# Kernel optimization log

Hardware: AMD Instinct MI355X
Metric: run time of the kernel (lower is better)

## Reference

```python
import jax, jax.numpy as jnp
import numpy as np

EMBED = 768
HEADS = 12
HEAD_DIM = EMBED // HEADS
HIDDEN = 4 * EMBED
EPS = 1e-5


def _layernorm(x, w, b):
    mu = jnp.mean(x, axis=-1, keepdims=True)
    var = jnp.mean(jnp.square(x - mu), axis=-1, keepdims=True)
    return (x - mu) * jax.lax.rsqrt(var + EPS) * w + b


def setup_inputs() -> dict:
    key = jax.random.key(0)
    ks = jax.random.split(key, 12)
    s = 0.02
    return {
        "x": jax.random.normal(ks[0], (2, 2048, EMBED), dtype=jnp.float32),
        "ln1_w": jnp.ones((EMBED,), jnp.float32),
        "ln1_b": jnp.zeros((EMBED,), jnp.float32),
        "qkv_w": jax.random.normal(ks[1], (3 * EMBED, EMBED), jnp.float32) * s,
        "qkv_b": jnp.zeros((3 * EMBED,), jnp.float32),
        "proj_w": jax.random.normal(ks[2], (EMBED, EMBED), jnp.float32) * s,
        "proj_b": jnp.zeros((EMBED,), jnp.float32),
        "ln2_w": jnp.ones((EMBED,), jnp.float32),
        "ln2_b": jnp.zeros((EMBED,), jnp.float32),
        "fc1_w": jax.random.normal(ks[3], (HIDDEN, EMBED), jnp.float32) * s,
        "fc1_b": jnp.zeros((HIDDEN,), jnp.float32),
        "fc2_w": jax.random.normal(ks[4], (EMBED, HIDDEN), jnp.float32) * s,
        "fc2_b": jnp.zeros((EMBED,), jnp.float32),
    }


def reference(x, ln1_w, ln1_b, qkv_w, qkv_b, proj_w, proj_b,
              ln2_w, ln2_b, fc1_w, fc1_b, fc2_w, fc2_b):
    B, N, C = x.shape
    scale = float(HEAD_DIM) ** 0.5  # NOTE: module MULTIPLIES by sqrt(head_dim)

    # --- attention branch ---
    h = _layernorm(x, ln1_w, ln1_b)
    qkv = h @ qkv_w.T + qkv_b                     # [B,N,3C]
    qkv = qkv.reshape(B, N, 3, HEADS, HEAD_DIM)
    q = qkv[:, :, 0].transpose(0, 2, 1, 3)        # [B,H,N,D]
    k = qkv[:, :, 1].transpose(0, 2, 1, 3)
    v = qkv[:, :, 2].transpose(0, 2, 1, 3)
    attn = jnp.einsum('bhnd,bhmd->bhnm', q, k) * scale
    attn = jax.nn.softmax(attn, axis=-1)
    o = jnp.einsum('bhnm,bhmd->bhnd', attn, v)    # [B,H,N,D]
    o = o.transpose(0, 2, 1, 3).reshape(B, N, C)
    x = x + (o @ proj_w.T + proj_b)

    # --- MLP branch ---
    h = _layernorm(x, ln2_w, ln2_b)
    h = jax.nn.gelu(h @ fc1_w.T + fc1_b, approximate=False)
    x = x + (h @ fc2_w.T + fc2_b)
    return x
```

## Files before the change

### kernel.cpp

```cpp
#include <hip/hip_runtime.h>
#include <hip/hip_bf16.h>

typedef __attribute__((ext_vector_type(8))) short short8;
typedef __attribute__((ext_vector_type(4))) float f32x4;
typedef __attribute__((ext_vector_type(4))) int i32x4;

__device__ inline unsigned short f2bs(float f) {
  union { float f; unsigned u; } v; v.f = f;
  unsigned r = v.u + 0x7fff + ((v.u >> 16) & 1);
  return (unsigned short)(r >> 16);
}

__device__ inline unsigned pkbf(float a, float b) {
  __hip_bfloat162 h = __float22bfloat162_rn(float2{a, b});
  union { __hip_bfloat162 h; unsigned u; } c; c.h = h;
  return c.u;
}

__device__ inline float exp2v(float x) {
  float r; asm("v_exp_f32 %0, %1" : "=v"(r) : "v"(x)); return r;
}

__device__ inline float max3f(float a, float b, float c) {
  return fmaxf(fmaxf(a, b), c);
}

__device__ inline void gload16(const void* g, void* l) {
  __builtin_amdgcn_global_load_lds((const __attribute__((address_space(1))) void*)g,
                                   (__attribute__((address_space(3))) void*)l,
                                   16, 0, 0);
}

__global__ __launch_bounds__(256)
void cvt_all(const float* __restrict__ s0, const float* __restrict__ s1,
             const float* __restrict__ s2, const float* __restrict__ s3,
             unsigned short* __restrict__ d0, unsigned short* __restrict__ d1,
             unsigned short* __restrict__ d2, unsigned short* __restrict__ d3)
{
  size_t i = (size_t)blockIdx.x * 256 + threadIdx.x;
  const float* src; unsigned short* dst;
  if (i < 442368) { src = s0; dst = d0; }
  else if (i < 589824) { src = s1; dst = d1; i -= 442368; }
  else if (i < 1179648) { src = s2; dst = d2; i -= 589824; }
  else { src = s3; dst = d3; i -= 1179648; }
  float4 v = ((const float4*)src)[i];
  ushort4 o;
  o.x = f2bs(v.x); o.y = f2bs(v.y); o.z = f2bs(v.z); o.w = f2bs(v.w);
  ((ushort4*)dst)[i] = o;
}

__global__ __launch_bounds__(256)
void ln_kernel(const float* __restrict__ x, const float* __restrict__ w,
               const float* __restrict__ bsh, unsigned short* __restrict__ out)
{
  const int row = blockIdx.x;
  const float* xr = x + (size_t)row * 768;
  float v[3];
  float s = 0.f, sq = 0.f;
#pragma unroll
  for (int i = 0; i < 3; ++i) {
    v[i] = xr[threadIdx.x + i * 256];
    s += v[i]; sq += v[i] * v[i];
  }
#pragma unroll
  for (int d = 1; d < 64; d <<= 1) {
    s  += __shfl_xor(s, d, 64);
    sq += __shfl_xor(sq, d, 64);
  }
  __shared__ float ss[4], ssq[4];
  const int wv = threadIdx.x >> 6;
  if ((threadIdx.x & 63) == 0) { ss[wv] = s; ssq[wv] = sq; }
  __syncthreads();
  s  = ss[0] + ss[1] + ss[2] + ss[3];
  sq = ssq[0] + ssq[1] + ssq[2] + ssq[3];
  const float mu = s * (1.0f / 768.0f);
  const float var = sq * (1.0f / 768.0f) - mu * mu;
  const float rstd = rsqrtf(var + 1e-5f);
#pragma unroll
  for (int i = 0; i < 3; ++i) {
    const int c = threadIdx.x + i * 256;
    out[(size_t)row * 768 + c] = f2bs((v[i] - mu) * rstd * w[c] + bsh[c]);
  }
}

__global__ __launch_bounds__(256)
void reduce_ln2(const float* __restrict__ p, const float* __restrict__ bias,
                const float* __restrict__ resid, const float* __restrict__ lw,
                const float* __restrict__ lb, float* __restrict__ x2,
                unsigned short* __restrict__ h)
{
  const size_t MN = 4096ull * 768;
  const int row = blockIdx.x;
  const size_t r0 = (size_t)row * 768;
  float v[3];
  float s = 0.f, sq = 0.f;
#pragma unroll
  for (int i = 0; i < 3; ++i) {
    const int c = threadIdx.x + i * 256;
    const float a = p[r0 + c] + p[MN + r0 + c] + bias[c] + resid[r0 + c];
    x2[r0 + c] = a;
    v[i] = a; s += a; sq += a * a;
  }
#pragma unroll
  for (int d = 1; d < 64; d <<= 1) {
    s  += __shfl_xor(s, d, 64);
    sq += __shfl_xor(sq, d, 64);
  }
  __shared__ float ss[4], ssq[4];
  const int wv = threadIdx.x >> 6;
  if ((threadIdx.x & 63) == 0) { ss[wv] = s; ssq[wv] = sq; }
  __syncthreads();
  s  = ss[0] + ss[1] + ss[2] + ss[3];
  sq = ssq[0] + ssq[1] + ssq[2] + ssq[3];
  const float mu = s * (1.0f / 768.0f);
  const float var = sq * (1.0f / 768.0f) - mu * mu;
  const float rstd = rsqrtf(var + 1e-5f);
#pragma unroll
  for (int i = 0; i < 3; ++i) {
    const int c = threadIdx.x + i * 256;
    h[r0 + c] = f2bs((v[i] - mu) * rstd * lw[c] + lb[c]);
  }
}

template<int S>
__global__ __launch_bounds__(256)
void reduce_k(const float* __restrict__ p, const float* __restrict__ bias,
              const float* __restrict__ resid, float* __restrict__ out)
{
  const size_t MN = 4096ull * 768;
  const size_t i = ((size_t)blockIdx.x * 256 + threadIdx.x) * 4;
  float4 a = *(const float4*)(p + i);
#pragma unroll
  for (int s = 1; s < S; ++s) {
    float4 b = *(const float4*)(p + s * MN + i);
    a.x += b.x; a.y += b.y; a.z += b.z; a.w += b.w;
  }
  const int col = (int)(i % 768);
  float4 bb = *(const float4*)(bias + col);
  float4 rr = *(const float4*)(resid + i);
  a.x += bb.x + rr.x; a.y += bb.y + rr.y; a.z += bb.z + rr.z; a.w += bb.w + rr.w;
  *(float4*)(out + i) = a;
}

template<int EPI>
__global__ __launch_bounds__(256, 3)
void gemm_nt(const unsigned short* __restrict__ A,
             const unsigned short* __restrict__ Bw,
             const float* __restrict__ bias,
             const float* __restrict__ resid,
             void* __restrict__ out0, void* __restrict__ out1, void* __restrict__ out2,
             int M, int N, int Kslice, int Kstride)
{
  __shared__ __align__(16) unsigned short As[3][128 * 32];
  __shared__ __align__(16) unsigned short Bs[3][128 * 32];
  const int tid = threadIdx.x;
  const int lane = tid & 63;
  const int w = tid >> 6;
  const int wr = w >> 1, wc = w & 1;
  const int l15 = lane & 15, g = lane >> 4;

  const int nwg = gridDim.x * gridDim.y;
  const int hw = blockIdx.y * gridDim.x + blockIdx.x;
  const int virt = (hw & 7) * (nwg >> 3) + (hw >> 3);
  const int m0 = (virt / gridDim.x) * 128;
  const int n0 = (virt % gridDim.x) * 128;
  const int kbase = blockIdx.z * Kslice;

  f32x4 acc[4][4];
#pragma unroll
  for (int m = 0; m < 4; ++m)
#pragma unroll
    for (int n = 0; n < 4; ++n)
      acc[m][n] = (f32x4){0.f, 0.f, 0.f, 0.f};

  auto stage = [&](int buf, int k0) {
#pragma unroll
    for (int i = 0; i < 2; ++i) {
      const int f = tid + i * 256;
      const int row = f >> 2, c8 = f & 3;
      const int sc = c8 ^ (row & 3);
      gload16(A  + (size_t)(m0 + row) * Kstride + kbase + k0 + sc * 8, (char*)&As[buf][0] + f * 16);
      gload16(Bw + (size_t)(n0 + row) * Kstride + kbase + k0 + sc * 8, (char*)&Bs[buf][0] + f * 16);
    }
  };

  const int NT = Kslice >> 5;
  stage(0, 0);
  stage(1, 32);

  for (int t = 0; t < NT; ++t) {
    const int buf = t % 3;
    if (t + 1 < NT) {
      asm volatile("s_waitcnt vmcnt(4)" ::: "memory");
    } else {
      asm volatile("s_waitcnt vmcnt(0)" ::: "memory");
    }
    __builtin_amdgcn_s_barrier();
    asm volatile("" ::: "memory");
    if (t + 2 < NT) stage((t + 2) % 3, (t + 2) * 32);

    short8 af[4], bfr[4];
#pragma unroll
    for (int m = 0; m < 4; ++m) {
      const int r = wr * 64 + m * 16 + l15;
      af[m] = *(const short8*)((const char*)&As[buf][0] + ((size_t)r * 32 + (g ^ (r & 3)) * 8) * 2);
    }
#pragma unroll
    for (int n = 0; n < 4; ++n) {
      const int r = wc * 64 + n * 16 + l15;
      bfr[n] = *(const short8*)((const char*)&Bs[buf][0] + ((size_t)r * 32 + (g ^ (r & 3)) * 8) * 2);
    }
#pragma unroll
    for (int m = 0; m < 4; ++m)
#pragma unroll
      for (int n = 0; n < 4; ++n)
        acc[m][n] = __builtin_amdgcn_mfma_f32_16x16x32_bf16(af[m], bfr[n], acc[m][n], 0, 0, 0);
    asm volatile("" ::: "memory");
  }

#pragma unroll
  for (int m = 0; m < 4; ++m) {
    const int gmBase = m0 + wr * 64 + m * 16 + g * 4;
#pragma unroll
    for (int n = 0; n < 4; ++n) {
      const int gn = n0 + wc * 64 + n * 16 + l15;
      const float bval = (EPI == 4) ? 0.0f : bias[gn];
      float vj[4];
#pragma unroll
      for (int j = 0; j < 4; ++j) vj[j] = acc[m][n][j] + bval;
      if (EPI == 0) {
        const int three = gn / 768;
        const int hh = (gn % 768) >> 6;
        const int d = gn & 63;
        const int bb = gmBase >> 11, t = gmBase & 2047;
        if (three == 2) {
          ushort4 pk;
          pk.x = f2bs(vj[0]); pk.y = f2bs(vj[1]); pk.z = f2bs(vj[2]); pk.w = f2bs(vj[3]);
          const int kt = t & 63;
          const size_t pos = ((((size_t)(bb * 12 + hh) * 32 + (t >> 6)) * 8 + (d >> 4) * 2 + (kt >> 5)) * 64
                              + ((kt >> 2) & 3) * 16 + (d & 15)) * 8 + ((kt >> 4) & 1) * 4;
          *(ushort4*)((unsigned short*)out2 + pos) = pk;
        } else {
          unsigned short* dst = (three == 0) ? (unsigned short*)out0 : (unsigned short*)out1;
#pragma unroll
          for (int j = 0; j < 4; ++j) {
            float v = vj[j];
            if (three == 0) v *= 11.5415603f;
            dst[(((size_t)bb * 12 + hh) * 2048 + (t + j)) * 64 + d] = f2bs(v);
          }
        }
      } else if (EPI == 1 || EPI == 3) {
#pragma unroll
        for (int j = 0; j < 4; ++j) {
          const int gm = gmBase + j;
          ((float*)out0)[(size_t)gm * N + gn] = vj[j] + resid[(size_t)gm * N + gn];
        }
      } else if (EPI == 2) {
#pragma unroll
        for (int j = 0; j < 4; ++j) {
          const int gm = gmBase + j;
          const float vv = vj[j];
          const float u = vv * (1.0f + 0.044715f * vv * vv);
          const float E = exp2v(2.0f * 0.7978845608f * 1.4426950409f * u);
          const float ge = vv - vv / (1.0f + E);
          ((unsigned short*)out0)[(size_t)gm * N + gn] = f2bs(ge);
        }
      } else {
        float* po = (float*)out0 + (size_t)blockIdx.z * M * N;
#pragma unroll
        for (int j = 0; j < 4; ++j) {
          const int gm = gmBase + j;
          po[(size_t)gm * N + gn] = vj[j];
        }
      }
    }
  }
}

template<int SPLIT>
__global__ __launch_bounds__(256, 6)
void attn_fwd(const unsigned short* __restrict__ Q,
              const unsigned short* __restrict__ K,
              const unsigned short* __restrict__ Vf,
              unsigned short* __restrict__ O,
              float* __restrict__ Op, float* __restrict__ Mb, float* __restrict__ Lb)
{
  __shared__ __align__(1024) unsigned short Ks[4096];
  __shared__ __align__(1024) unsigned short Vs[2][4096];
  const int tid = threadIdx.x, lane = tid & 63, w = tid >> 6;
  const int l15 = lane & 15, g = lane >> 4;

  const int hw = blockIdx.y * gridDim.x + blockIdx.x;
  const int virt = (hw & 7) * 96 + (hw >> 3);
  const int qblk = virt & 31;
  const int bh = virt >> 5;
  const int b = bh / 12, h = bh % 12;
  const int q0 = qblk * 64;
  const int half = SPLIT ? blockIdx.z : 0;
  const int NT = SPLIT ? 16 : 32;
  const int T0 = half * 16;
  const unsigned short* Qb = Q  + (size_t)bh * 2048 * 64;
  const unsigned short* Kb = K  + (size_t)bh * 2048 * 64;
  const unsigned short* Vb = Vf + (size_t)bh * 2048 * 64;

  const int qr = q0 + w * 16 + l15;
  short8 qf[2];
  qf[0] = *(const short8*)(Qb + (size_t)qr * 64 + g * 8);
  qf[1] = *(const short8*)(Qb + (size_t)qr * 64 + 32 + g * 8);

  float m_run = -1e30f, l_part = 0.f;
  f32x4 o_acc[4];
#pragma unroll
  for (int dc = 0; dc < 4; ++dc) o_acc[dc] = (f32x4){0.f, 0.f, 0.f, 0.f};

  auto stageK = [&](int gt) {
    const int kb = gt * 64;
#pragma unroll
    for (int i = 0; i < 2; ++i) {
      const int f = w * 2 + i;
      const int n = f >> 1, kc = f & 1;
      gload16(Kb + (size_t)(kb + n * 16 + l15) * 64 + kc * 32 + g * 8,
              (char*)&Ks[0] + f * 1024);
    }
  };
  auto stageV = [&](int buf, int gt) {
#pragma unroll
    for (int i = 0; i < 2; ++i) {
      const int chunk = tid + i * 256;
      gload16(Vb + (size_t)gt * 4096 + chunk * 8,
              (char*)&Vs[buf][0] + chunk * 16);
    }
  };

  stageK(T0);
  stageV(0, T0);

  for (int t = 0; t < NT; ++t) {
    const int vbuf = t & 1;
    asm volatile("s_waitcnt vmcnt(0)" ::: "memory");
    __builtin_amdgcn_s_barrier();
    asm volatile("" ::: "memory");
    if (t + 1 < NT) stageV(vbuf ^ 1, T0 + t + 1);

    f32x4 s2[4];
#pragma unroll
    for (int n = 0; n < 4; ++n) s2[n] = (f32x4){0.f, 0.f, 0.f, 0.f};
    __builtin_amdgcn_s_setprio(1);
#pragma unroll
    for (int n = 0; n < 4; ++n) {
      short8 kf0 = *(const short8*)(&Ks[(n * 2 + 0) * 512 + lane * 8]);
      short8 kf1 = *(const short8*)(&Ks[(n * 2 + 1) * 512 + lane * 8]);
      s2[n] = __builtin_amdgcn_mfma_f32_16x16x32_bf16(kf0, qf[0], s2[n], 0, 0, 0);
      s2[n] = __builtin_amdgcn_mfma_f32_16x16x32_bf16(kf1, qf[1], s2[n], 0, 0, 0);
    }
    __builtin_amdgcn_s_setprio(0);

    asm volatile("" ::: "memory");
    __builtin_amdgcn_s_barrier();
    asm volatile("" ::: "memory");
    if (t + 1 < NT) stageK(T0 + t + 1);

    float mx = max3f(max3f(s2[0][0], s2[0][1], s2[0][2]),
                     max3f(s2[0][3], s2[1][0], s2[1][1]),
                     max3f(s2[1][2], s2[1][3], s2[2][0]));
    mx = max3f(mx, max3f(s2[2][1], s2[2][2], s2[2][3]),
                   max3f(s2[3][0], s2[3][1], fmaxf(s2[3][2], s2[3][3])));
    mx = fmaxf(mx, __shfl_xor(mx, 16, 64));
    mx = fmaxf(mx, __shfl_xor(mx, 32, 64));
    if (__any(mx > m_run + 8.0f)) {
      const float mn = fmaxf(m_run, mx);
      const float alpha = exp2v(m_run - mn);
      m_run = mn;
      l_part *= alpha;
#pragma unroll
      for (int j = 0; j < 4; ++j) {
        const float aB = __shfl(alpha, (lane & 48) | (g * 4 + j), 64);
#pragma unroll
        for (int dc = 0; dc < 4; ++dc) o_acc[dc][j] *= aB;
      }
    }
    float e[4][4];
    float rs = 0.f;
#pragma unroll
    for (int n = 0; n < 4; ++n)
#pragma unroll
      for (int j = 0; j < 4; ++j) {
        e[n][j] = exp2v(s2[n][j] - m_run);
        rs += e[n][j];
      }
    l_part += rs;

    unsigned pw[2][4];
#pragma unroll
    for (int kc = 0; kc < 2; ++kc) {
      pw[kc][0] = pkbf(e[2 * kc][0],     e[2 * kc][1]);
      pw[kc][1] = pkbf(e[2 * kc][2],     e[2 * kc][3]);
      pw[kc][2] = pkbf(e[2 * kc + 1][0], e[2 * kc + 1][1]);
      pw[kc][3] = pkbf(e[2 * kc + 1][2], e[2 * kc + 1][3]);
    }

    const char* vsb = (const char*)&Vs[vbuf][0];
    __builtin_amdgcn_s_setprio(1);
#pragma unroll
    for (int kc = 0; kc < 2; ++kc) {
      i32x4 pt; pt.x = (int)pw[kc][0]; pt.y = (int)pw[kc][1]; pt.z = (int)pw[kc][2]; pt.w = (int)pw[kc][3];
      short8 pf = *(short8*)&pt;
#pragma unroll
      for (int dc = 0; dc < 4; ++dc) {
        short8 vfr = *(const short8*)(vsb + (((dc * 2 + kc) * 64 + lane) * 16));
        o_acc[dc] = __builtin_amdgcn_mfma_f32_16x16x32_bf16(pf, vfr, o_acc[dc], 0, 0, 0);
      }
    }
    __builtin_amdgcn_s_setprio(0);
    asm volatile("" ::: "memory");
  }

  l_part += __shfl_xor(l_part, 16, 64);
  l_part += __shfl_xor(l_part, 32, 64);
  if (SPLIT) {
    const int rowBase = (half * 24 + bh) * 2048;
    if (g == 0) {
      const int qm = q0 + w * 16 + l15;
      Mb[rowBase + qm] = m_run;
      Lb[rowBase + qm] = l_part;
    }
#pragma unroll
    for (int j = 0; j < 4; ++j) {
      const int row = q0 + w * 16 + g * 4 + j;
#pragma unroll
      for (int dc = 0; dc < 4; ++dc)
        Op[(size_t)(rowBase + row) * 64 + dc * 16 + l15] = o_acc[dc][j];
    }
  } else {
#pragma unroll
    for (int j = 0; j < 4; ++j) {
      const float lB = __shfl(l_part, (lane & 48) | (g * 4 + j), 64);
      const float inv = 1.0f / lB;
      const int qrow = q0 + w * 16 + g * 4 + j;
#pragma unroll
      for (int dc = 0; dc < 4; ++dc)
        O[((size_t)b * 2048 + qrow) * 768 + h * 64 + dc * 16 + l15] = f2bs(o_acc[dc][j] * inv);
    }
  }
}

__global__ __launch_bounds__(256)
void attn_combine(const float* __restrict__ Op, const float* __restrict__ Mb,
                  const float* __restrict__ Lb, unsigned short* __restrict__ O)
{
  const int idx = blockIdx.x * 256 + threadIdx.x;
  const int e4 = idx * 4;
  const int row = e4 >> 6;
  const int d0 = e4 & 63;
  const float m1 = Mb[row], m2 = Mb[49152 + row];
  const float l1 = Lb[row], l2 = Lb[49152 + row];
  const float mm = fmaxf(m1, m2);
  const float w1 = exp2v(m1 - mm), w2 = exp2v(m2 - mm);
  const float inv = 1.0f / (l1 * w1 + l2 * w2);
  const float4 o1 = *(const float4*)(Op + (size_t)row * 64 + d0);
  const float4 o2 = *(const float4*)(Op + 49152ull * 64 + (size_t)row * 64 + d0);
  ushort4 r;
  r.x = f2bs((o1.x * w1 + o2.x * w2) * inv);
  r.y = f2bs((o1.y * w1 + o2.y * w2) * inv);
  r.z = f2bs((o1.z * w1 + o2.z * w2) * inv);
  r.w = f2bs((o1.w * w1 + o2.w * w2) * inv);
  const int bh = row >> 11, q = row & 2047;
  const int b = bh / 12, hh = bh % 12;
  *(ushort4*)(O + ((size_t)(b * 2048 + q)) * 768 + hh * 64 + d0) = r;
}

extern "C" void kernel_launch(void* const* d_in, const int* in_sizes, int n_in,
                              void* d_out, int out_size, void* d_ws, size_t ws_size,
                              hipStream_t stream)
{
  const float* x      = (const float*)d_in[0];
  const float* ln1_w  = (const float*)d_in[1];
  const float* ln1_b  = (const float*)d_in[2];
  const float* qkv_w  = (const float*)d_in[3];
  const float* qkv_b  = (const float*)d_in[4];
  const float* proj_w = (const float*)d_in[5];
  const float* proj_b = (const float*)d_in[6];
  const float* ln2_w  = (const float*)d_in[7];
  const float* ln2_b  = (const float*)d_in[8];
  const float* fc1_w  = (const float*)d_in[9];
  const float* fc1_b  = (const float*)d_in[10];
  const float* fc2_w  = (const float*)d_in[11];
  const float* fc2_b  = (const float*)d_in[12];

  char* base = (char*)d_ws;
  size_t off = 0;
  auto take = [&](size_t bytes) {
    void* r = base + off;
    off = (off + bytes + 255) & ~(size_t)255;
    return r;
  };
  unsigned short* wq = (unsigned short*)take(2304ull * 768 * 2);
  unsigned short* wp = (unsigned short*)take(768ull * 768 * 2);
  unsigned short* w1 = (unsigned short*)take(3072ull * 768 * 2);
  unsigned short* w2 = (unsigned short*)take(768ull * 3072 * 2);
  unsigned short* h  = (unsigned short*)take(4096ull * 768 * 2);
  float* x2          = (float*)take(4096ull * 768 * 4);
  char* big          = (char*)take(4096ull * 3072 * 2);
  unsigned short* Qb = (unsigned short*)big;
  unsigned short* Kb = (unsigned short*)(big + 4096ull * 768 * 2);
  unsigned short* Vb = (unsigned short*)(big + 2ull * 4096 * 768 * 2);
  unsigned short* a2 = (unsigned short*)big;
  float* part        = (float*)take(4ull * 4096 * 768 * 4);
  float* Mb_         = (float*)take(2ull * 49152 * 4);
  float* Lb_         = (float*)take(2ull * 49152 * 4);
  const bool can_split = off <= ws_size;

  cvt_all<<<6912, 256, 0, stream>>>(qkv_w, proj_w, fc1_w, fc2_w, wq, wp, w1, w2);

  ln_kernel<<<4096, 256, 0, stream>>>(x, ln1_w, ln1_b, h);
  gemm_nt<0><<<dim3(18, 32), 256, 0, stream>>>(h, wq, qkv_b, nullptr, Qb, Kb, Vb, 4096, 2304, 768, 768);

  if (can_split) {
    attn_fwd<1><<<dim3(32, 24, 2), 256, 0, stream>>>(Qb, Kb, Vb, nullptr, part, Mb_, Lb_);
    attn_combine<<<3072, 256, 0, stream>>>(part, Mb_, Lb_, h);
  } else {
    attn_fwd<0><<<dim3(32, 24), 256, 0, stream>>>(Qb, Kb, Vb, h, nullptr, nullptr, nullptr);
  }

  if (can_split) {
    gemm_nt<4><<<dim3(6, 32, 2), 256, 0, stream>>>(h, wp, nullptr, nullptr, part, nullptr, nullptr, 4096, 768, 384, 768);
    reduce_ln2<<<4096, 256, 0, stream>>>(part, proj_b, x, ln2_w, ln2_b, x2, h);
  } else {
    gemm_nt<1><<<dim3(6, 32), 256, 0, stream>>>(h, wp, proj_b, x, x2, nullptr, nullptr, 4096, 768, 768, 768);
    ln_kernel<<<4096, 256, 0, stream>>>(x2, ln2_w, ln2_b, h);
  }

  gemm_nt<2><<<dim3(24, 32), 256, 0, stream>>>(h, w1, fc1_b, nullptr, a2, nullptr, nullptr, 4096, 3072, 768, 768);

  if (can_split) {
    gemm_nt<4><<<dim3(6, 32, 4), 256, 0, stream>>>(a2, w2, nullptr, nullptr, part, nullptr, nullptr, 4096, 768, 768, 3072);
    reduce_k<4><<<3072, 256, 0, stream>>>(part, fc2_b, x2, (float*)d_out);
  } else {
    gemm_nt<3><<<dim3(6, 32), 256, 0, stream>>>(a2, w2, fc2_b, x2, d_out, nullptr, nullptr, 4096, 768, 3072, 3072);
  }
}
```

Measured before the change: 197.6 us.

## Store split-K and split-attention partials in bf16 and relayout GEMM LDS tiles

Split-K GEMM partials and split-KV attention partial outputs are now written and read as bf16 instead of fp32, halving the intermediate traffic through the workspace. The reduce, reduce_ln2 and combine kernels convert those bf16 partials back to float before summing. GEMM shared-memory staging is also changed to a fragment-major layout: each 16-row chunk is stored contiguously in 1KB, so every lane reads 16 bytes at lane*16 with no swizzle. The trade-off is extra rounding error on the partial sums, and the new LDS layout may bring back bank conflicts on the async global-to-LDS writes.

Result: slower. 220.6 us (+11.6%).

```diff
diff --git a/kernel.cpp b/kernel.cpp
--- a/kernel.cpp
+++ b/kernel.cpp
@@ -9,6 +9,10 @@
   union { float f; unsigned u; } v; v.f = f;
   unsigned r = v.u + 0x7fff + ((v.u >> 16) & 1);
   return (unsigned short)(r >> 16);
+}
+
+__device__ inline float bs2f(unsigned short u) {
+  union { unsigned u; float f; } c; c.u = (unsigned)u << 16; return c.f;
 }
 
 __device__ inline unsigned pkbf(float a, float b) {
@@ -84,7 +88,7 @@
 }
 
 __global__ __launch_bounds__(256)
-void reduce_ln2(const float* __restrict__ p, const float* __restrict__ bias,
+void reduce_ln2(const unsigned short* __restrict__ p, const float* __restrict__ bias,
                 const float* __restrict__ resid, const float* __restrict__ lw,
                 const float* __restrict__ lb, float* __restrict__ x2,
                 unsigned short* __restrict__ h)
@@ -97,7 +101,7 @@
 #pragma unroll
   for (int i = 0; i < 3; ++i) {
     const int c = threadIdx.x + i * 256;
-    const float a = p[r0 + c] + p[MN + r0 + c] + bias[c] + resid[r0 + c];
+    const float a = bs2f(p[r0 + c]) + bs2f(p[MN + r0 + c]) + bias[c] + resid[r0 + c];
     x2[r0 + c] = a;
     v[i] = a; s += a; sq += a * a;
   }
@@ -124,22 +128,24 @@
 
 template<int S>
 __global__ __launch_bounds__(256)
-void reduce_k(const float* __restrict__ p, const float* __restrict__ bias,
+void reduce_k(const unsigned short* __restrict__ p, const float* __restrict__ bias,
               const float* __restrict__ resid, float* __restrict__ out)
 {
   const size_t MN = 4096ull * 768;
   const size_t i = ((size_t)blockIdx.x * 256 + threadIdx.x) * 4;
-  float4 a = *(const float4*)(p + i);
-#pragma unroll
-  for (int s = 1; s < S; ++s) {
-    float4 b = *(const float4*)(p + s * MN + i);
-    a.x += b.x; a.y += b.y; a.z += b.z; a.w += b.w;
+  float ax = 0.f, ay = 0.f, az = 0.f, aw = 0.f;
+#pragma unroll
+  for (int s = 0; s < S; ++s) {
+    ushort4 b = *(const ushort4*)(p + s * MN + i);
+    ax += bs2f(b.x); ay += bs2f(b.y); az += bs2f(b.z); aw += bs2f(b.w);
   }
   const int col = (int)(i % 768);
   float4 bb = *(const float4*)(bias + col);
   float4 rr = *(const float4*)(resid + i);
-  a.x += bb.x + rr.x; a.y += bb.y + rr.y; a.z += bb.z + rr.z; a.w += bb.w + rr.w;
-  *(float4*)(out + i) = a;
+  float4 r;
+  r.x = ax + bb.x + rr.x; r.y = ay + bb.y + rr.y;
+  r.z = az + bb.z + rr.z; r.w = aw + bb.w + rr.w;
+  *(float4*)(out + i) = r;
 }
 
 template<int EPI>
@@ -151,8 +157,8 @@
              void* __restrict__ out0, void* __restrict__ out1, void* __restrict__ out2,
              int M, int N, int Kslice, int Kstride)
 {
-  __shared__ __align__(16) unsigned short As[3][128 * 32];
-  __shared__ __align__(16) unsigned short Bs[3][128 * 32];
+  __shared__ __align__(1024) unsigned short As[3][4096];
+  __shared__ __align__(1024) unsigned short Bs[3][4096];
   const int tid = threadIdx.x;
   const int lane = tid & 63;
   const int w = tid >> 6;
@@ -176,11 +182,11 @@
   auto stage = [&](int buf, int k0) {
 #pragma unroll
     for (int i = 0; i < 2; ++i) {
-      const int f = tid + i * 256;
-      const int row = f >> 2, c8 = f & 3;
-      const int sc = c8 ^ (row & 3);
-      gload16(A  + (size_t)(m0 + row) * Kstride + kbase + k0 + sc * 8, (char*)&As[buf][0] + f * 16);
-      gload16(Bw + (size_t)(n0 + row) * Kstride + kbase + k0 + sc * 8, (char*)&Bs[buf][0] + f * 16);
+      const int f = w * 2 + i;
+      gload16(A  + (size_t)(m0 + f * 16 + l15) * Kstride + kbase + k0 + g * 8,
+              (char*)&As[buf][0] + f * 1024);
+      gload16(Bw + (size_t)(n0 + f * 16 + l15) * Kstride + kbase + k0 + g * 8,
+              (char*)&Bs[buf][0] + f * 1024);
     }
   };
 
@@ -201,15 +207,11 @@
 
     short8 af[4], bfr[4];
 #pragma unroll
-    for (int m = 0; m < 4; ++m) {
-      const int r = wr * 64 + m * 16 + l15;
-      af[m] = *(const short8*)((const char*)&As[buf][0] + ((size_t)r * 32 + (g ^ (r & 3)) * 8) * 2);
-    }
-#pragma unroll
-    for (int n = 0; n < 4; ++n) {
-      const int r = wc * 64 + n * 16 + l15;
-      bfr[n] = *(const short8*)((const char*)&Bs[buf][0] + ((size_t)r * 32 + (g ^ (r & 3)) * 8) * 2);
-    }
+    for (int m = 0; m < 4; ++m)
+      af[m] = *(const short8*)((const char*)&As[buf][0] + (wr * 4 + m) * 1024 + lane * 16);
+#pragma unroll
+    for (int n = 0; n < 4; ++n)
+      bfr[n] = *(const short8*)((const char*)&Bs[buf][0] + (wc * 4 + n) * 1024 + lane * 16);
 #pragma unroll
     for (int m = 0; m < 4; ++m)
 #pragma unroll
@@ -266,11 +268,11 @@
           ((unsigned short*)out0)[(size_t)gm * N + gn] = f2bs(ge);
         }
       } else {
-        float* po = (float*)out0 + (size_t)blockIdx.z * M * N;
+        unsigned short* po = (unsigned short*)out0 + (size_t)blockIdx.z * M * N;
 #pragma unroll
         for (int j = 0; j < 4; ++j) {
           const int gm = gmBase + j;
-          po[(size_t)gm * N + gn] = vj[j];
+          po[(size_t)gm * N + gn] = f2bs(vj[j]);
         }
       }
     }
@@ -283,7 +285,7 @@
               const unsigned short* __restrict__ K,
               const unsigned short* __restrict__ Vf,
               unsigned short* __restrict__ O,
-              float* __restrict__ Op, float* __restrict__ Mb, float* __restrict__ Lb)
+              unsigned short* __restrict__ Op, float* __restrict__ Mb, float* __restrict__ Lb)
 {
   __shared__ __align__(1024) unsigned short Ks[4096];
   __shared__ __align__(1024) unsigned short Vs[2][4096];
@@ -429,7 +431,7 @@
       const int row = q0 + w * 16 + g * 4 + j;
 #pragma unroll
       for (int dc = 0; dc < 4; ++dc)
-        Op[(size_t)(rowBase + row) * 64 + dc * 16 + l15] = o_acc[dc][j];
+        Op[(size_t)(rowBase + row) * 64 + dc * 16 + l15] = f2bs(o_acc[dc][j]);
     }
   } else {
 #pragma unroll
@@ -445,7 +447,7 @@
 }
 
 __global__ __launch_bounds__(256)
-void attn_combine(const float* __restrict__ Op, const float* __restrict__ Mb,
+void attn_combine(const unsigned short* __restrict__ Op, const float* __restrict__ Mb,
                   const float* __restrict__ Lb, unsigned short* __restrict__ O)
 {
   const int idx = blockIdx.x * 256 + threadIdx.x;
@@ -457,13 +459,13 @@
   const float mm = fmaxf(m1, m2);
   const float w1 = exp2v(m1 - mm), w2 = exp2v(m2 - mm);
   const float inv = 1.0f / (l1 * w1 + l2 * w2);
-  const float4 o1 = *(const float4*)(Op + (size_t)row * 64 + d0);
-  const float4 o2 = *(const float4*)(Op + 49152ull * 64 + (size_t)row * 64 + d0);
+  ushort4 a1 = *(const ushort4*)(Op + (size_t)row * 64 + d0);
+  ushort4 a2 = *(const ushort4*)(Op + 49152ull * 64 + (size_t)row * 64 + d0);
   ushort4 r;
-  r.x = f2bs((o1.x * w1 + o2.x * w2) * inv);
-  r.y = f2bs((o1.y * w1 + o2.y * w2) * inv);
-  r.z = f2bs((o1.z * w1 + o2.z * w2) * inv);
-  r.w = f2bs((o1.w * w1 + o2.w * w2) * inv);
+  r.x = f2bs((bs2f(a1.x) * w1 + bs2f(a2.x) * w2) * inv);
+  r.y = f2bs((bs2f(a1.y) * w1 + bs2f(a2.y) * w2) * inv);
+  r.z = f2bs((bs2f(a1.z) * w1 + bs2f(a2.z) * w2) * inv);
+  r.w = f2bs((bs2f(a1.w) * w1 + bs2f(a2.w) * w2) * inv);
   const int bh = row >> 11, q = row & 2047;
   const int b = bh / 12, hh = bh % 12;
   *(ushort4*)(O + ((size_t)(b * 2048 + q)) * 768 + hh * 64 + d0) = r;
@@ -505,7 +507,7 @@
   unsigned short* Kb = (unsigned short*)(big + 4096ull * 768 * 2);
   unsigned short* Vb = (unsigned short*)(big + 2ull * 4096 * 768 * 2);
   unsigned short* a2 = (unsigned short*)big;
-  float* part        = (float*)take(4ull * 4096 * 768 * 4);
+  unsigned short* part = (unsigned short*)take(4ull * 4096 * 768 * 2);
   float* Mb_         = (float*)take(2ull * 49152 * 4);
   float* Lb_         = (float*)take(2ull * 49152 * 4);
   const bool can_split = off <= ws_size;
```
